# Kernel tuning notes

Hardware: AMD Instinct MI355X
Metric: run time of the kernel (lower is better)

## Reference

```python
import jax, jax.numpy as jnp
import numpy as np

B, D, E, H, L = 16384, 512, 16, 256, 64
NOISE_EPS = 0.01


def setup_inputs() -> dict:
    key = jax.random.key(0)
    ks = jax.random.split(key, 8)
    s = 0.05
    return {
        "x": jax.random.normal(ks[0], (B, D), dtype=jnp.float32),
        "noise": jax.random.normal(ks[1], (B, E), dtype=jnp.float32),
        "w_gate": jax.random.normal(ks[2], (D, E), dtype=jnp.float32) * s,
        "w_noise": jax.random.normal(ks[3], (D, E), dtype=jnp.float32) * s,
        "W1": jax.random.normal(ks[4], (E, D, H), dtype=jnp.float32) * s,
        "b1": jnp.zeros((E, H), dtype=jnp.float32),
        "W2": jax.random.normal(ks[5], (E, H, L), dtype=jnp.float32) * s,
        "b2": jnp.zeros((E, L), dtype=jnp.float32),
    }


def _noisy_gating(x, noise, w_gate, w_noise):
    clean_logits = x @ w_gate                                   # [B, E]
    noise_stddev = jax.nn.softplus(x @ w_noise) + NOISE_EPS     # [B, E]
    logits = jax.nn.softmax(clean_logits + noise * noise_stddev, axis=1)
    mean_weight = jnp.mean(logits, axis=-1) - 1e-8              # [B]
    gates = jnp.where(logits >= mean_weight[:, None], logits, 0.0)
    gates = gates / jnp.sum(gates, axis=-1, keepdims=True)
    return gates


def reference(x, noise, w_gate, w_noise, W1, b1, W2, b2):
    gates = _noisy_gating(x, noise, w_gate, w_noise)            # [B, E]
    # Dense equivalent of SparseDispatcher dispatch -> expert MLP -> combine:
    # combine scatters expert_e(x[b]) * gates[b,e] into slot (b, e), zeros elsewhere;
    # since gates==0 at masked slots, this equals gates[:,:,None] * all-expert outputs.
    h = jnp.tanh(jnp.einsum("bd,edh->beh", x, W1) + b1[None])   # [B, E, H]
    y = jnp.einsum("beh,ehl->bel", h, W2) + b2[None]            # [B, E, L]
    return gates[:, :, None] * y                                # [B, E, L]
```

## Files before the change

### kernel.cpp

```cpp
#include <hip/hip_runtime.h>
#include <stdint.h>

#define BROWS 16384
#define DDIM  512
#define EEXP  16
#define HDIM  256
#define LDIM  64
#define BM    64

typedef __bf16  bf16x8  __attribute__((ext_vector_type(8)));
typedef float   floatx4 __attribute__((ext_vector_type(4)));
typedef ushort  ushort8 __attribute__((ext_vector_type(8)));
typedef unsigned int u32;

__device__ __forceinline__ ushort f2bf(float f) {
    uint32_t u = __builtin_bit_cast(uint32_t, f);
    u += 0x7fffu + ((u >> 16) & 1u);
    return (ushort)(u >> 16);
}

__device__ __forceinline__ float fast_tanh(float x) {
    float e = __builtin_amdgcn_exp2f(x * 2.8853900817779268f);
    return 1.0f - 2.0f * __builtin_amdgcn_rcpf(e + 1.0f);
}

__device__ __forceinline__ void gl_lds16(const void* g, void* l) {
    __builtin_amdgcn_global_load_lds(
        (const __attribute__((address_space(1))) u32*)g,
        (__attribute__((address_space(3))) u32*)l, 16, 0, 0);
}

__global__ __launch_bounds__(256) void gate_aux_kernel(
    const float* __restrict__ x,
    const float* __restrict__ noise,
    const float* __restrict__ wg,
    const float* __restrict__ wn,
    const float* __restrict__ W1,
    const float* __restrict__ W2,
    float* __restrict__ gates,
    ushort* __restrict__ xbf,
    ushort* __restrict__ W1T,
    ushort* __restrict__ W2T,
    u32* __restrict__ cnt,
    u32* __restrict__ rowlist,
    float* __restrict__ out)
{
    if (blockIdx.x >= 512) {
        __shared__ float tile[32][33];
        int b = blockIdx.x - 512;
        const float* src; ushort* dst; int R, C, c0, r0, swz, ei;
        if (b < 2048) {
            ei = b >> 7; int rem = b & 127;
            c0 = (rem & 7) * 32; r0 = (rem >> 3) * 32;
            R = DDIM; C = HDIM; swz = 1;
            src = W1; dst = W1T;
        } else {
            b -= 2048;
            ei = b >> 4; int rem = b & 15;
            c0 = (rem & 1) * 32; r0 = (rem >> 1) * 32;
            R = HDIM; C = LDIM; swz = 0;
            src = W2; dst = W2T;
        }
        const int tx = threadIdx.x & 31, ty = threadIdx.x >> 5;
        const float* s = src + (size_t)ei * R * C;
        ushort* d = dst + (size_t)ei * R * C;

        #pragma unroll
        for (int i = 0; i < 4; ++i) {
            int rr = ty + i * 8;
            tile[rr][tx] = s[(size_t)(r0 + rr) * C + c0 + tx];
        }
        __syncthreads();
        #pragma unroll
        for (int i = 0; i < 4; ++i) {
            int cc = ty + i * 8;
            int h = c0 + cc;
            int col = r0 + tx;
            int col2 = col;
            if (swz) {
                int g = (col >> 3) & 7;
                col2 = (col & ~63) | ((g ^ (h & 7)) << 3) | (col & 7);
            }
            d[(size_t)h * R + col2] = f2bf(tile[tx][cc]);
        }
        return;
    }

    __shared__ __align__(16) float xs[32 * 132];
    __shared__ __align__(16) float wTg[16 * 132];
    __shared__ __align__(16) float wTn[16 * 132];
    __shared__ u32 lcnt[16];
    __shared__ u32 lbase[16];
    __shared__ ushort lrows[16 * 32];
    __shared__ u32 izn;
    __shared__ ushort izlist[512];

    const int t    = threadIdx.x;
    const int blk  = blockIdx.x;
    const int row0 = blk * 32;
    const int og   = t & 15, rg = t >> 4;

    if (t < 16) lcnt[t] = 0;
    if (t == 0) izn = 0;

    floatx4 accg4[2] = {}, accn4[2] = {};

    for (int ch = 0; ch < 4; ++ch) {
        const int k0 = ch * 128;
        __syncthreads();
        {
            int r = t >> 3, c = (t & 7) * 16;
            const float* src = &x[(size_t)(row0 + r) * DDIM + k0 + c];
            float4 f[4];
            #pragma unroll
            for (int i = 0; i < 4; ++i)
                f[i] = reinterpret_cast<const float4*>(src)[i];
            float* dst = &xs[r * 132 + c];
            #pragma unroll
            for (int i = 0; i < 4; ++i)
                reinterpret_cast<float4*>(dst)[i] = f[i];

            const int row = row0 + r;
            const int sw  = r & 7;
            #pragma unroll
            for (int i = 0; i < 2; ++i) {
                int cb = k0 + c + i * 8;
                int kb = cb >> 6;
                int g  = (cb >> 3) & 7;
                int gp = g ^ sw;
                float4 a = f[i * 2], b = f[i * 2 + 1];
                ushort8 t8;
                t8[0]=f2bf(a.x); t8[1]=f2bf(a.y); t8[2]=f2bf(a.z); t8[3]=f2bf(a.w);
                t8[4]=f2bf(b.x); t8[5]=f2bf(b.y); t8[6]=f2bf(b.z); t8[7]=f2bf(b.w);
                *reinterpret_cast<ushort8*>(&xbf[(size_t)row * DDIM + kb * 64 + gp * 8]) = t8;
            }
        }
        {
            int d = t >> 1, e0 = (t & 1) * 8;
            float4 a0 = *reinterpret_cast<const float4*>(&wg[(size_t)(k0 + d) * EEXP + e0]);
            float4 a1 = *reinterpret_cast<const float4*>(&wg[(size_t)(k0 + d) * EEXP + e0 + 4]);
            float4 b0 = *reinterpret_cast<const float4*>(&wn[(size_t)(k0 + d) * EEXP + e0]);
            float4 b1 = *reinterpret_cast<const float4*>(&wn[(size_t)(k0 + d) * EEXP + e0 + 4]);
            wTg[(e0+0)*132+d]=a0.x; wTg[(e0+1)*132+d]=a0.y; wTg[(e0+2)*132+d]=a0.z; wTg[(e0+3)*132+d]=a0.w;
            wTg[(e0+4)*132+d]=a1.x; wTg[(e0+5)*132+d]=a1.y; wTg[(e0+6)*132+d]=a1.z; wTg[(e0+7)*132+d]=a1.w;
            wTn[(e0+0)*132+d]=b0.x; wTn[(e0+1)*132+d]=b0.y; wTn[(e0+2)*132+d]=b0.z; wTn[(e0+3)*132+d]=b0.w;
            wTn[(e0+4)*132+d]=b1.x; wTn[(e0+5)*132+d]=b1.y; wTn[(e0+6)*132+d]=b1.z; wTn[(e0+7)*132+d]=b1.w;
        }
        __syncthreads();

        #pragma unroll 8
        for (int d4 = 0; d4 < 32; ++d4) {
            floatx4 wgv = *reinterpret_cast<const floatx4*>(&wTg[og * 132 + d4 * 4]);
            floatx4 wnv = *reinterpret_cast<const floatx4*>(&wTn[og * 132 + d4 * 4]);
            #pragma unroll
            for (int rr = 0; rr < 2; ++rr) {
                floatx4 xv = *reinterpret_cast<const floatx4*>(&xs[(rg * 2 + rr) * 132 + d4 * 4]);
                accg4[rr] += xv * wgv;
                accn4[rr] += xv * wnv;
            }
        }
    }

    #pragma unroll
    for (int rr = 0; rr < 2; ++rr) {
        const int row = row0 + rg * 2 + rr;
        float accg = accg4[rr][0] + accg4[rr][1] + accg4[rr][2] + accg4[rr][3];
        float accn = accn4[rr][0] + accn4[rr][1] + accn4[rr][2] + accn4[rr][3];

        float sp = fmaxf(accn, 0.f) + log1pf(expf(-fabsf(accn)));
        float stddev = sp + 0.01f;
        float nz = noise[(size_t)row * EEXP + og];
        float z = accg + nz * stddev;

        float m = z;
        #pragma unroll
        for (int mask = 8; mask >= 1; mask >>= 1)
            m = fmaxf(m, __shfl_xor(m, mask, 16));
        float ez = expf(z - m);
        float s = ez;
        #pragma unroll
        for (int mask = 8; mask >= 1; mask >>= 1)
            s += __shfl_xor(s, mask, 16);
        float logit = ez / s;

        float lsum = logit;
        #pragma unroll
        for (int mask = 8; mask >= 1; mask >>= 1)
            lsum += __shfl_xor(lsum, mask, 16);
        float mean = lsum * (1.0f / 16.0f) - 1e-8f;

        float gate = (logit >= mean) ? logit : 0.0f;
        float denom = gate;
        #pragma unroll
        for (int mask = 8; mask >= 1; mask >>= 1)
            denom += __shfl_xor(denom, mask, 16);

        gates[(size_t)row * EEXP + og] = gate / denom;

        if (gate > 0.0f) {
            u32 p = atomicAdd(&lcnt[og], 1u);
            lrows[og * 32 + p] = (ushort)(rg * 2 + rr);
        } else {
            u32 p = atomicAdd(&izn, 1u);
            izlist[p] = (ushort)((rg * 2 + rr) * 16 + og);
        }
    }

    __syncthreads();
    if (t < 16) lbase[t] = atomicAdd(&cnt[t], lcnt[t]);

    {
        const u32 ni = izn;
        const int grp = t >> 4, l16 = t & 15;
        float4* o4 = reinterpret_cast<float4*>(out);
        const float4 zf = {0.f, 0.f, 0.f, 0.f};
        for (u32 i = grp; i < ni; i += 16) {
            int slot = izlist[i];
            int rl = slot >> 4, e = slot & 15;
            o4[(size_t)(row0 + rl) * 256 + e * 16 + l16] = zf;
        }
    }

    __syncthreads();
    for (int i = t; i < 16 * 32; i += 256) {
        int e = i >> 5, j = i & 31;
        if ((u32)j < lcnt[e])
            rowlist[(size_t)e * BROWS + lbase[e] + j] = row0 + lrows[e * 32 + j];
    }
}

__global__ __launch_bounds__(256, 4) void expert_kernel(
    const ushort* __restrict__ xbf,
    const float*  __restrict__ gates,
    const ushort* __restrict__ W1T,
    const float*  __restrict__ b1,
    const ushort* __restrict__ W2T,
    const float*  __restrict__ b2,
    const u32*    __restrict__ cnt,
    const u32*    __restrict__ rowlist,
    float* __restrict__ out)
{
    __shared__ __align__(16) ushort lds[20480];

    const int bx = blockIdx.x;
    const int e  = bx & 15;
    const int t  = bx >> 4;

    const int count = (int)cnt[e];
    if (t * BM >= count) return;
    const int nrt = min(BM, count - t * BM);
    const u32* rl = rowlist + (size_t)e * BROWS + t * BM;

    const int tid  = threadIdx.x;
    const int lane = tid & 63;
    const int wave = tid >> 6;

    const int lr = lane & 15;
    const int q  = lane >> 4;
    const int kq = q * 8;
    const int rq = q * 4;
    const int la = lane >> 3, lb = lane & 7;

    const char* xg = (const char*)xbf;
    const char* w1 = (const char*)W1T + (size_t)e * HDIM * 1024;

    size_t abase[2]; int sxr[2];
    #pragma unroll
    for (int p = 0; p < 2; ++p) {
        int r  = wave * 16 + p * 8 + la;
        int rc = min(r, nrt - 1);
        u32 ri = rl[rc];
        abase[p] = (size_t)ri * 1024;
        sxr[p]   = (la ^ (int)(ri & 7)) << 4;
    }

    floatx4 acc[4][4] = {};

    for (int kb = 0; kb < 8; ++kb) {
        const int koff = kb * 128;
        #pragma unroll
        for (int p = 0; p < 2; ++p) {
            int c = wave * 2 + p;
            gl_lds16(xg + abase[p] + koff + ((lb << 4) ^ sxr[p]), &lds[c * 512]);
        }
        #pragma unroll
        for (int p = 0; p < 8; ++p) {
            int c = wave * 8 + p;
            gl_lds16(w1 + (size_t)(c * 8 + la) * 1024 + koff + (lb << 4),
                     &lds[4096 + c * 512]);
        }
        __syncthreads();

        #pragma unroll
        for (int s = 0; s < 2; ++s) {
            const int g = s * 4 + q;
            bf16x8 af[4], bfr[4];
            #pragma unroll
            for (int i = 0; i < 4; ++i) {
                int r = i * 16 + lr;
                af[i] = *reinterpret_cast<const bf16x8*>(&lds[r * 64 + ((g ^ (r & 7)) << 3)]);
            }
            #pragma unroll
            for (int j = 0; j < 4; ++j) {
                int r = wave * 64 + j * 16 + lr;
                bfr[j] = *reinterpret_cast<const bf16x8*>(&lds[4096 + r * 64 + ((g ^ (r & 7)) << 3)]);
            }
            #pragma unroll
            for (int i = 0; i < 4; ++i)
                #pragma unroll
                for (int j = 0; j < 4; ++j)
                    acc[i][j] = __builtin_amdgcn_mfma_f32_16x16x32_bf16(
                        af[i], bfr[j], acc[i][j], 0, 0, 0);
        }
        __syncthreads();
    }

    float b1v[4];
    #pragma unroll
    for (int j = 0; j < 4; ++j)
        b1v[j] = b1[e * HDIM + wave * 64 + j * 16 + lr];

    #pragma unroll
    for (int i = 0; i < 4; ++i)
        #pragma unroll
        for (int j = 0; j < 4; ++j) {
            int c = wave * 64 + j * 16 + lr;
            int gg = c >> 3;
            #pragma unroll
            for (int rr = 0; rr < 4; ++rr) {
                int r = i * 16 + rq + rr;
                float v = fast_tanh(acc[i][j][rr] + b1v[j]);
                lds[r * 256 + (((gg & 24) | ((gg & 7) ^ (r & 7))) << 3) + (c & 7)] = f2bf(v);
            }
        }
    __syncthreads();

    const ushort* w2 = W2T + (size_t)e * LDIM * HDIM;
    floatx4 acc2[4] = {};
    #pragma unroll
    for (int s = 0; s < 8; ++s) {
        int r = wave * 16 + lr;
        int g = s * 4 + q;
        bf16x8 af = *reinterpret_cast<const bf16x8*>(
            &lds[r * 256 + (((g & 24) | ((g & 7) ^ (r & 7))) << 3)]);
        #pragma unroll
        for (int j = 0; j < 4; ++j) {
            bf16x8 bfr = *reinterpret_cast<const bf16x8*>(
                &w2[(size_t)(j * 16 + lr) * HDIM + s * 32 + kq]);
            acc2[j] = __builtin_amdgcn_mfma_f32_16x16x32_bf16(af, bfr, acc2[j], 0, 0, 0);
        }
    }

    float b2v[4];
    #pragma unroll
    for (int j = 0; j < 4; ++j)
        b2v[j] = b2[e * LDIM + j * 16 + lr];

    #pragma unroll
    for (int rr = 0; rr < 4; ++rr) {
        int r  = wave * 16 + rq + rr;
        int rc = min(r, nrt - 1);
        u32 ri = rl[rc];
        float gsc = gates[(size_t)ri * EEXP + e];
        if (r < nrt) {
            #pragma unroll
            for (int j = 0; j < 4; ++j)
                out[(size_t)ri * (EEXP * LDIM) + e * LDIM + j * 16 + lr] =
                    (acc2[j][rr] + b2v[j]) * gsc;
        }
    }
}

extern "C" void kernel_launch(void* const* d_in, const int* in_sizes, int n_in,
                              void* d_out, int out_size, void* d_ws, size_t ws_size,
                              hipStream_t stream) {
    (void)in_sizes; (void)n_in; (void)out_size; (void)ws_size;
    const float* x     = (const float*)d_in[0];
    const float* noise = (const float*)d_in[1];
    const float* wg    = (const float*)d_in[2];
    const float* wn    = (const float*)d_in[3];
    const float* W1    = (const float*)d_in[4];
    const float* b1    = (const float*)d_in[5];
    const float* W2    = (const float*)d_in[6];
    const float* b2    = (const float*)d_in[7];
    float* out = (float*)d_out;

    char* ws = (char*)d_ws;
    float*  gates   = (float*)ws;
    ushort* W1T     = (ushort*)(ws + (1 << 20));
    ushort* W2T     = (ushort*)(ws + (5 << 20));
    ushort* xbf     = (ushort*)(ws + (6 << 20));
    u32*    cnt     = (u32*)(ws + (22 << 20));
    u32*    rowlist = (u32*)(ws + (24 << 20));

    hipMemsetAsync(cnt, 0, EEXP * sizeof(u32), stream);
    gate_aux_kernel<<<512 + 2304, 256, 0, stream>>>(
        x, noise, wg, wn, W1, W2, gates, xbf, W1T, W2T, cnt, rowlist, out);
    expert_kernel<<<(BROWS / BM) * EEXP, 256, 0, stream>>>(
        xbf, gates, W1T, b1, W2T, b2, cnt, rowlist, out);
}
```

Before: 171.9 us.

## Double-buffer gating loads and enlarge weight-transpose tiles to 64x64

The gating part now prefetches the next 128-wide chunk of x and the gate weights into registers while the current chunk is in shared memory. Two shared buffers let it drop one barrier per chunk. The weight transpose/bf16 conversion blocks now handle 64x64 tiles with float4 loads and ushort4 stores, which cuts the transpose block count from 2304 to 576. This raises shared memory per block (one large shared array) and register use, which may lower occupancy.

After: 170.8 us, median of 2. No clear change (-0.6%).

```diff
diff --git a/kernel.cpp b/kernel.cpp
--- a/kernel.cpp
+++ b/kernel.cpp
@@ -45,116 +45,142 @@
     u32* __restrict__ rowlist,
     float* __restrict__ out)
 {
-    if (blockIdx.x >= 512) {
-        __shared__ float tile[32][33];
-        int b = blockIdx.x - 512;
-        const float* src; ushort* dst; int R, C, c0, r0, swz, ei;
-        if (b < 2048) {
-            ei = b >> 7; int rem = b & 127;
-            c0 = (rem & 7) * 32; r0 = (rem >> 3) * 32;
-            R = DDIM; C = HDIM; swz = 1;
-            src = W1; dst = W1T;
-        } else {
-            b -= 2048;
-            ei = b >> 4; int rem = b & 15;
-            c0 = (rem & 1) * 32; r0 = (rem >> 1) * 32;
-            R = HDIM; C = LDIM; swz = 0;
-            src = W2; dst = W2T;
-        }
-        const int tx = threadIdx.x & 31, ty = threadIdx.x >> 5;
-        const float* s = src + (size_t)ei * R * C;
-        ushort* d = dst + (size_t)ei * R * C;
-
-        #pragma unroll
-        for (int i = 0; i < 4; ++i) {
-            int rr = ty + i * 8;
-            tile[rr][tx] = s[(size_t)(r0 + rr) * C + c0 + tx];
-        }
-        __syncthreads();
-        #pragma unroll
-        for (int i = 0; i < 4; ++i) {
-            int cc = ty + i * 8;
-            int h = c0 + cc;
-            int col = r0 + tx;
-            int col2 = col;
-            if (swz) {
-                int g = (col >> 3) & 7;
-                col2 = (col & ~63) | ((g ^ (h & 7)) << 3) | (col & 7);
-            }
-            d[(size_t)h * R + col2] = f2bf(tile[tx][cc]);
-        }
-        return;
-    }
-
-    __shared__ __align__(16) float xs[32 * 132];
-    __shared__ __align__(16) float wTg[16 * 132];
-    __shared__ __align__(16) float wTn[16 * 132];
+    __shared__ __align__(16) float smbig[16896];
     __shared__ u32 lcnt[16];
     __shared__ u32 lbase[16];
     __shared__ ushort lrows[16 * 32];
     __shared__ u32 izn;
     __shared__ ushort izlist[512];
 
+    if (blockIdx.x >= 512) {
+        float (*tile)[68] = reinterpret_cast<float(*)[68]>(smbig);
+        int b = blockIdx.x - 512;
+        const float* src; ushort* dst; int R, C, c0, r0, swz, ei;
+        if (b < 512) {
+            ei = b >> 5; int rem = b & 31;
+            r0 = (rem >> 2) * 64; c0 = (rem & 3) * 64;
+            R = DDIM; C = HDIM; swz = 1;
+            src = W1; dst = W1T;
+        } else {
+            b -= 512;
+            ei = b >> 2; int rem = b & 3;
+            r0 = rem * 64; c0 = 0;
+            R = HDIM; C = LDIM; swz = 0;
+            src = W2; dst = W2T;
+        }
+        const int tr  = threadIdx.x >> 2;
+        const int tc4 = threadIdx.x & 3;
+
+        const float* s = src + (size_t)ei * R * C + (size_t)(r0 + tr) * C + c0 + tc4 * 16;
+        #pragma unroll
+        for (int i = 0; i < 4; ++i) {
+            float4 v = *reinterpret_cast<const float4*>(s + i * 4);
+            *reinterpret_cast<float4*>(&tile[tr][tc4 * 16 + i * 4]) = v;
+        }
+        __syncthreads();
+
+        ushort* d = dst + (size_t)ei * R * C;
+        const int hh = c0 + tr;
+        #pragma unroll
+        for (int i = 0; i < 4; ++i) {
+            int rrb  = tc4 * 16 + i * 4;
+            int colb = r0 + rrb;
+            int col2 = colb;
+            if (swz) {
+                int g = (colb >> 3) & 7;
+                col2 = (colb & ~63) | ((g ^ (hh & 7)) << 3) | (colb & 7);
+            }
+            ushort4 o;
+            o.x = f2bf(tile[rrb + 0][tr]);
+            o.y = f2bf(tile[rrb + 1][tr]);
+            o.z = f2bf(tile[rrb + 2][tr]);
+            o.w = f2bf(tile[rrb + 3][tr]);
+            *reinterpret_cast<ushort4*>(&d[(size_t)hh * R + col2]) = o;
+        }
+        return;
+    }
+
+    float* xs  = smbig;
+    float* wtg = smbig + 2 * 32 * 132;
+    float* wtn = wtg   + 2 * 16 * 132;
+
     const int t    = threadIdx.x;
     const int blk  = blockIdx.x;
     const int row0 = blk * 32;
     const int og   = t & 15, rg = t >> 4;
+    const int sr   = t >> 3, sc = (t & 7) * 16;
+    const int sd   = t >> 1, se = (t & 1) * 8;
 
     if (t < 16) lcnt[t] = 0;
     if (t == 0) izn = 0;
 
+    float4 xf0, xf1, xf2, xf3, wg0, wg1, wn0, wn1;
+    const float* srcx0 = &x[(size_t)(row0 + sr) * DDIM + sc];
+
+    {
+        const float4* p = reinterpret_cast<const float4*>(srcx0);
+        xf0 = p[0]; xf1 = p[1]; xf2 = p[2]; xf3 = p[3];
+        const float4* pg = reinterpret_cast<const float4*>(&wg[(size_t)sd * EEXP + se]);
+        const float4* pn = reinterpret_cast<const float4*>(&wn[(size_t)sd * EEXP + se]);
+        wg0 = pg[0]; wg1 = pg[1]; wn0 = pn[0]; wn1 = pn[1];
+    }
+
     floatx4 accg4[2] = {}, accn4[2] = {};
 
     for (int ch = 0; ch < 4; ++ch) {
-        const int k0 = ch * 128;
-        __syncthreads();
+        const int k0  = ch * 128;
+        const int buf = ch & 1;
+        float* xsb = xs  + buf * (32 * 132);
+        float* wgl = wtg + buf * (16 * 132);
+        float* wnl = wtn + buf * (16 * 132);
+
         {
-            int r = t >> 3, c = (t & 7) * 16;
-            const float* src = &x[(size_t)(row0 + r) * DDIM + k0 + c];
-            float4 f[4];
-            #pragma unroll
-            for (int i = 0; i < 4; ++i)
-                f[i] = reinterpret_cast<const float4*>(src)[i];
-            float* dst = &xs[r * 132 + c];
-            #pragma unroll
-            for (int i = 0; i < 4; ++i)
-                reinterpret_cast<float4*>(dst)[i] = f[i];
-
-            const int row = row0 + r;
-            const int sw  = r & 7;
+            float* dstx = &xsb[sr * 132 + sc];
+            reinterpret_cast<float4*>(dstx)[0] = xf0;
+            reinterpret_cast<float4*>(dstx)[1] = xf1;
+            reinterpret_cast<float4*>(dstx)[2] = xf2;
+            reinterpret_cast<float4*>(dstx)[3] = xf3;
+
+            const int row = row0 + sr;
+            const int sw  = sr & 7;
             #pragma unroll
             for (int i = 0; i < 2; ++i) {
-                int cb = k0 + c + i * 8;
+                int cb = k0 + sc + i * 8;
                 int kb = cb >> 6;
                 int g  = (cb >> 3) & 7;
                 int gp = g ^ sw;
-                float4 a = f[i * 2], b = f[i * 2 + 1];
+                float4 a = (i == 0) ? xf0 : xf2;
+                float4 b = (i == 0) ? xf1 : xf3;
                 ushort8 t8;
                 t8[0]=f2bf(a.x); t8[1]=f2bf(a.y); t8[2]=f2bf(a.z); t8[3]=f2bf(a.w);
                 t8[4]=f2bf(b.x); t8[5]=f2bf(b.y); t8[6]=f2bf(b.z); t8[7]=f2bf(b.w);
                 *reinterpret_cast<ushort8*>(&xbf[(size_t)row * DDIM + kb * 64 + gp * 8]) = t8;
             }
-        }
-        {
-            int d = t >> 1, e0 = (t & 1) * 8;
-            float4 a0 = *reinterpret_cast<const float4*>(&wg[(size_t)(k0 + d) * EEXP + e0]);
-            float4 a1 = *reinterpret_cast<const float4*>(&wg[(size_t)(k0 + d) * EEXP + e0 + 4]);
-            float4 b0 = *reinterpret_cast<const float4*>(&wn[(size_t)(k0 + d) * EEXP + e0]);
-            float4 b1 = *reinterpret_cast<const float4*>(&wn[(size_t)(k0 + d) * EEXP + e0 + 4]);
-            wTg[(e0+0)*132+d]=a0.x; wTg[(e0+1)*132+d]=a0.y; wTg[(e0+2)*132+d]=a0.z; wTg[(e0+3)*132+d]=a0.w;
-            wTg[(e0+4)*132+d]=a1.x; wTg[(e0+5)*132+d]=a1.y; wTg[(e0+6)*132+d]=a1.z; wTg[(e0+7)*132+d]=a1.w;
-            wTn[(e0+0)*132+d]=b0.x; wTn[(e0+1)*132+d]=b0.y; wTn[(e0+2)*132+d]=b0.z; wTn[(e0+3)*132+d]=b0.w;
-            wTn[(e0+4)*132+d]=b1.x; wTn[(e0+5)*132+d]=b1.y; wTn[(e0+6)*132+d]=b1.z; wTn[(e0+7)*132+d]=b1.w;
-        }
+
+            wgl[(se+0)*132+sd]=wg0.x; wgl[(se+1)*132+sd]=wg0.y; wgl[(se+2)*132+sd]=wg0.z; wgl[(se+3)*132+sd]=wg0.w;
+            wgl[(se+4)*132+sd]=wg1.x; wgl[(se+5)*132+sd]=wg1.y; wgl[(se+6)*132+sd]=wg1.z; wgl[(se+7)*132+sd]=wg1.w;
+            wnl[(se+0)*132+sd]=wn0.x; wnl[(se+1)*132+sd]=wn0.y; wnl[(se+2)*132+sd]=wn0.z; wnl[(se+3)*132+sd]=wn0.w;
+            wnl[(se+4)*132+sd]=wn1.x; wnl[(se+5)*132+sd]=wn1.y; wnl[(se+6)*132+sd]=wn1.z; wnl[(se+7)*132+sd]=wn1.w;
+        }
+
+        if (ch < 3) {
+            const int k1 = k0 + 128;
+            const float4* p = reinterpret_cast<const float4*>(srcx0 + k1);
+            xf0 = p[0]; xf1 = p[1]; xf2 = p[2]; xf3 = p[3];
+            const float4* pg = reinterpret_cast<const float4*>(&wg[(size_t)(k1 + sd) * EEXP + se]);
+            const float4* pn = reinterpret_cast<const float4*>(&wn[(size_t)(k1 + sd) * EEXP + se]);
+            wg0 = pg[0]; wg1 = pg[1]; wn0 = pn[0]; wn1 = pn[1];
+        }
+
         __syncthreads();
 
         #pragma unroll 8
         for (int d4 = 0; d4 < 32; ++d4) {
-            floatx4 wgv = *reinterpret_cast<const floatx4*>(&wTg[og * 132 + d4 * 4]);
-            floatx4 wnv = *reinterpret_cast<const floatx4*>(&wTn[og * 132 + d4 * 4]);
+            floatx4 wgv = *reinterpret_cast<const floatx4*>(&wgl[og * 132 + d4 * 4]);
+            floatx4 wnv = *reinterpret_cast<const floatx4*>(&wnl[og * 132 + d4 * 4]);
             #pragma unroll
             for (int rr = 0; rr < 2; ++rr) {
-                floatx4 xv = *reinterpret_cast<const floatx4*>(&xs[(rg * 2 + rr) * 132 + d4 * 4]);
+                floatx4 xv = *reinterpret_cast<const floatx4*>(&xsb[(rg * 2 + rr) * 132 + d4 * 4]);
                 accg4[rr] += xv * wgv;
                 accn4[rr] += xv * wnv;
             }
@@ -394,7 +420,7 @@
     u32*    rowlist = (u32*)(ws + (24 << 20));
 
     hipMemsetAsync(cnt, 0, EEXP * sizeof(u32), stream);
-    gate_aux_kernel<<<512 + 2304, 256, 0, stream>>>(
+    gate_aux_kernel<<<512 + 576, 256, 0, stream>>>(
         x, noise, wg, wn, W1, W2, gates, xbf, W1T, W2T, cnt, rowlist, out);
     expert_kernel<<<(BROWS / BM) * EEXP, 256, 0, stream>>>(
         xbf, gates, W1T, b1, W2T, b2, cnt, rowlist, out);
```
